# Performance work log

Measured on AMD Instinct MI355X. Metric: run time of the kernel, lower is better.

## Reference

```python
import jax, jax.numpy as jnp
import numpy as np

K = 16  # number of nearest neighbors (excluding self)
N = 16384


def setup_inputs() -> dict:
    key = jax.random.key(0)
    nodes = jax.random.normal(key, (N, 3), dtype=jnp.float32)
    return {"nodes": nodes}


def reference(nodes):
    n = nodes.shape[0]
    # Pairwise Euclidean distances via the Gram trick:
    # d(i,j)^2 = |x_i|^2 + |x_j|^2 - 2 <x_i, x_j>
    sq = jnp.sum(nodes * nodes, axis=1)                      # [n]
    d2 = sq[:, None] + sq[None, :] - 2.0 * (nodes @ nodes.T)  # [n, n]
    dist = jnp.sqrt(jnp.maximum(d2, 0.0))                    # clamp fp noise
    # k+1 smallest per row (self is nearest with distance ~0), then drop self.
    _, idx = jax.lax.top_k(-dist, K + 1)                     # ascending distance
    idx = idx[:, 1:]                                         # [n, K]
    rows = jnp.arange(n)[:, None]                            # [n, 1]
    adjacency = jnp.zeros((n, n), dtype=jnp.float32).at[rows, idx].set(1.0)
    return adjacency
```

## Files before the change

kernel.cpp:

```cpp
#include <hip/hip_runtime.h>
#include <math.h>

#define NN 16384
#define KK 16
#define RPW 4
#define SW 4
#define RPB (SW * RPW)
#define CAP 512
#define NB 1024
#define NT 64
#define FILL_BLOCKS 2048
#define SCAN_BLOCKS (NN / RPB)

typedef float f32x4 __attribute__((ext_vector_type(4)));
typedef unsigned long long u64;
typedef unsigned short u16;

#define WS_PTS   0
#define WS_PERM  (NN * 16)
#define WS_HIST  (WS_PERM + NN * 4)
#define WS_CUR   (WS_HIST + NB * 4)
#define WS_TMM   (WS_CUR + NB * 4)
#define WS_NB    (WS_TMM + NT * 8)
#define WS_NEED  (WS_NB + (size_t)NN * KK * 2)

__global__ void zero_hist(int* __restrict__ hist) { hist[threadIdx.x] = 0; }

__device__ __forceinline__ int xbucket(float x) {
    int b = (int)((x + 6.0f) * (NB / 12.0f));
    return b < 0 ? 0 : (b > NB - 1 ? NB - 1 : b);
}

__global__ void hist_kernel(const float* __restrict__ nodes, int* __restrict__ hist) {
    const int i = blockIdx.x * 256 + threadIdx.x;
    atomicAdd(&hist[xbucket(nodes[3 * i])], 1);
}

__global__ void scan_kernel(const int* __restrict__ hist, int* __restrict__ cur) {
    __shared__ int s[NB];
    const int tid = threadIdx.x;
    const int h0 = hist[tid];
    s[tid] = h0; __syncthreads();
    for (int o = 1; o < NB; o <<= 1) {
        const int v = (tid >= o) ? s[tid - o] : 0;
        __syncthreads();
        s[tid] += v;
        __syncthreads();
    }
    cur[tid] = s[tid] - h0;
}

__global__ void scatter_kernel(const float* __restrict__ nodes, int* __restrict__ cur,
                               float4* __restrict__ pts, int* __restrict__ perm) {
#pragma clang fp contract(off)
    const int i = blockIdx.x * 256 + threadIdx.x;
    const float x = nodes[3 * i], y = nodes[3 * i + 1], z = nodes[3 * i + 2];
    const float sq = (x * x + y * y) + z * z;
    const int pos = atomicAdd(&cur[xbucket(x)], 1);
    pts[pos] = make_float4(x, y, z, sq);
    perm[pos] = i;
}

__global__ void bounds_kernel(const float4* __restrict__ pts, float2* __restrict__ tmm) {
    __shared__ float mn[256], mx[256];
    const int tid = threadIdx.x;
    const float x = pts[blockIdx.x * 256 + tid].x;
    mn[tid] = x; mx[tid] = x; __syncthreads();
    for (int o = 128; o >= 1; o >>= 1) {
        if (tid < o) { mn[tid] = fminf(mn[tid], mn[tid + o]); mx[tid] = fmaxf(mx[tid], mx[tid + o]); }
        __syncthreads();
    }
    if (tid == 0) tmm[blockIdx.x] = make_float2(mn[0], mx[0]);
}

__device__ __forceinline__ float bcastf(float v, int l) {
    return __int_as_float(__builtin_amdgcn_readlane(__float_as_int(v), l));
}
__device__ __forceinline__ bool lexless(float da, int ia, float db, int ib) {
    return (da < db) || ((da == db) && (ia < ib));
}
__device__ __forceinline__ void insert_tile(bool rough, float d2, int j,
                                            float& ld, int& li,
                                            float& td, int& ti, float& td2u,
                                            int lane) {
#pragma clang fp contract(off)
    if (!__any(rough)) return;
    float dist = INFINITY;
    if (rough) dist = sqrtf(fmaxf(d2, 0.0f));
    bool done = false;
    while (true) {
        const bool pass = (!done) && rough && lexless(dist, j, td, ti);
        const u64 m = __ballot(pass);
        if (m == 0ull) break;
        const int src = __ffsll(m) - 1;
        const float dc = __shfl(dist, src);
        const int   ic = __shfl(j, src);
        if (lane == src) done = true;
        const bool gt = lexless(dc, ic, ld, li);
        const u64 gm = __ballot(gt);
        const int p = __ffsll(gm) - 1;
        const float pd = __shfl_up(ld, 1);
        const int   pi = __shfl_up(li, 1);
        if (gt) {
            if (lane == p) { ld = dc; li = ic; }
            else           { ld = pd; li = pi; }
        }
        td = __shfl(ld, 16);
        ti = __shfl(li, 16);
        td2u = td * td * 1.000001f;
    }
}

__device__ __forceinline__ void scan_body(int sblock,
                                          const float4* __restrict__ pts,
                                          const int* __restrict__ perm,
                                          const int* __restrict__ cur,
                                          const float2* __restrict__ tmm_g,
                                          const float* __restrict__ nodes,
                                          float* __restrict__ out,
                                          u16* __restrict__ nbws) {
#pragma clang fp contract(off)
    const int lane = threadIdx.x & 63;
    const int wid  = threadIdx.x >> 6;
    const int tid  = threadIdx.x;
    const int rowBase = sblock * RPB;

    __shared__ float2 tmm[NT];
    __shared__ u16 buf[SW][RPW][CAP];
    __shared__ u64 sel[SW][CAP];
    __shared__ int cnt[SW][RPW];

    if (tid < NT) tmm[tid] = tmm_g[tid];
    __syncthreads();

    float xs[RPW], ys[RPW], zs[RPW], ss[RPW];
    int tc[RPW];
#pragma unroll
    for (int r = 0; r < RPW; ++r) {
        const int row = rowBase + wid * RPW + r;
        xs[r] = nodes[3 * row];
        ys[r] = nodes[3 * row + 1];
        zs[r] = nodes[3 * row + 2];
        ss[r] = (xs[r] * xs[r] + ys[r] * ys[r]) + zs[r] * zs[r];
        int t = (cur[xbucket(xs[r])] - 1) >> 8;
        t = t - 1; t = t < 0 ? 0 : (t > NT - 3 ? NT - 3 : t);
        tc[r] = t;
    }

    float rm[RPW];
#pragma unroll
    for (int r = 0; r < RPW; ++r) rm[r] = INFINITY;
#pragma unroll
    for (int r = 0; r < RPW; ++r) {
        for (int tt = 0; tt < 3; ++tt) {
            const int tb = (tc[r] + tt) * 256;
            const float4 q0 = pts[tb + lane];
            const float4 q1 = pts[tb + 64 + lane];
            const float4 q2 = pts[tb + 128 + lane];
            const float4 q3 = pts[tb + 192 + lane];
            const float d0 = (ss[r] + q0.w) - 2.0f * fmaf(zs[r], q0.z, fmaf(ys[r], q0.y, xs[r] * q0.x));
            const float d1 = (ss[r] + q1.w) - 2.0f * fmaf(zs[r], q1.z, fmaf(ys[r], q1.y, xs[r] * q1.x));
            const float d2 = (ss[r] + q2.w) - 2.0f * fmaf(zs[r], q2.z, fmaf(ys[r], q2.y, xs[r] * q2.x));
            const float d3 = (ss[r] + q3.w) - 2.0f * fmaf(zs[r], q3.z, fmaf(ys[r], q3.y, xs[r] * q3.x));
            rm[r] = fminf(rm[r], fminf(fminf(d0, d1), fminf(d2, d3)));
        }
    }
    float sv[RPW];
#pragma unroll
    for (int r = 0; r < RPW; ++r) sv[r] = rm[r];
#pragma unroll
    for (int k = 2; k <= 64; k <<= 1) {
#pragma unroll
        for (int j = k >> 1; j >= 1; j >>= 1) {
            const bool keepmin = (((lane & j) == 0) == ((lane & k) == 0));
#pragma unroll
            for (int r = 0; r < RPW; ++r) {
                const float o = __shfl_xor(sv[r], j);
                sv[r] = keepmin ? fminf(sv[r], o) : fmaxf(sv[r], o);
            }
        }
    }
    float tau[RPW];
#pragma unroll
    for (int r = 0; r < RPW; ++r)
        tau[r] = fmaxf(bcastf(sv[r], 16), 0.0f) * 1.000002f + 1e-30f;

    if (lane < RPW) cnt[wid][lane] = 0;
    asm volatile("s_waitcnt lgkmcnt(0)" ::: "memory");

    for (int t = 0; t < NT; ++t) {
        const float2 mm = tmm[t];
        bool kp[RPW]; bool anyk = false;
#pragma unroll
        for (int r = 0; r < RPW; ++r) {
            const float dx = fmaxf(fmaxf(mm.x - xs[r], xs[r] - mm.y), 0.0f);
            kp[r] = (dx * dx <= tau[r] * 1.00001f + 5e-5f);
            anyk |= kp[r];
        }
        if (!anyk) continue;
        const int base = t * 256;
        const float4 q0 = pts[base + lane];
        const float4 q1 = pts[base + 64 + lane];
        const float4 q2 = pts[base + 128 + lane];
        const float4 q3 = pts[base + 192 + lane];
#pragma unroll
        for (int r = 0; r < RPW; ++r) {
            if (!kp[r]) continue;
            const float d0 = (ss[r] + q0.w) - 2.0f * fmaf(zs[r], q0.z, fmaf(ys[r], q0.y, xs[r] * q0.x));
            const float d1 = (ss[r] + q1.w) - 2.0f * fmaf(zs[r], q1.z, fmaf(ys[r], q1.y, xs[r] * q1.x));
            const float d2 = (ss[r] + q2.w) - 2.0f * fmaf(zs[r], q2.z, fmaf(ys[r], q2.y, xs[r] * q2.x));
            const float d3 = (ss[r] + q3.w) - 2.0f * fmaf(zs[r], q3.z, fmaf(ys[r], q3.y, xs[r] * q3.x));
            const bool p0 = d0 <= tau[r], p1 = d1 <= tau[r];
            const bool p2 = d2 <= tau[r], p3 = d3 <= tau[r];
            if (p0 | p1 | p2 | p3) {
                if (p0) { const int o = atomicAdd(&cnt[wid][r], 1);
                          if (o < CAP) buf[wid][r][o] = (u16)(base + lane); }
                if (p1) { const int o = atomicAdd(&cnt[wid][r], 1);
                          if (o < CAP) buf[wid][r][o] = (u16)(base + 64 + lane); }
                if (p2) { const int o = atomicAdd(&cnt[wid][r], 1);
                          if (o < CAP) buf[wid][r][o] = (u16)(base + 128 + lane); }
                if (p3) { const int o = atomicAdd(&cnt[wid][r], 1);
                          if (o < CAP) buf[wid][r][o] = (u16)(base + 192 + lane); }
            }
        }
    }
    asm volatile("s_waitcnt lgkmcnt(0)" ::: "memory");

#pragma unroll
    for (int r = 0; r < RPW; ++r) {
        const int C = cnt[wid][r];
        const int row = rowBase + wid * RPW + r;
        if (C <= CAP) {
            for (int e = lane; e < C; e += 64) {
                const int si = (int)buf[wid][r][e];
                const float4 q = pts[si];
                const float dd = (ss[r] + q.w) - 2.0f * fmaf(zs[r], q.z, fmaf(ys[r], q.y, xs[r] * q.x));
                const float dist = sqrtf(fmaxf(dd, 0.0f));
                sel[wid][e] = (((u64)__float_as_uint(dist)) << 32) | (unsigned)perm[si];
            }
            asm volatile("s_waitcnt lgkmcnt(0) vmcnt(0)" ::: "memory");
            for (int e = lane; e < C; e += 64) {
                const u64 my = sel[wid][e];
                int rk = 0;
                for (int c = 0; c < C; ++c)
                    rk += (sel[wid][c] < my) ? 1 : 0;
                if (rk >= 1 && rk <= KK) {
                    if (nbws) nbws[(size_t)row * KK + rk - 1] = (u16)(my & 0xffffu);
                    else      out[(size_t)row * NN + (int)(my & 0xffffffffu)] = 1.0f;
                }
            }
            asm volatile("s_waitcnt lgkmcnt(0)" ::: "memory");
        } else {
            float ld = INFINITY; int li = 0x7fffffff;
            float td = INFINITY; int ti = 0x7fffffff; float t2 = INFINITY;
            for (int tt = 0; tt < NN / 64; ++tt) {
                const int j = tt * 64 + lane;
                const float4 q = pts[j];
                const int oi = perm[j];
                const float dd = (ss[r] + q.w) - 2.0f * fmaf(zs[r], q.z, fmaf(ys[r], q.y, xs[r] * q.x));
                insert_tile(dd <= t2, dd, oi, ld, li, td, ti, t2, lane);
            }
            if (lane >= 1 && lane <= KK) {
                if (nbws) nbws[(size_t)row * KK + lane - 1] = (u16)li;
                else      out[(size_t)row * NN + li] = 1.0f;
            }
        }
    }
}

__global__ __launch_bounds__(256) void mega_kernel(const float4* __restrict__ pts,
                                                   const int* __restrict__ perm,
                                                   const int* __restrict__ cur,
                                                   const float2* __restrict__ tmm_g,
                                                   const float* __restrict__ nodes,
                                                   float* __restrict__ out,
                                                   u16* __restrict__ nbws) {
    const int b = blockIdx.x;
    if (b % 3 != 0) {
        const int fidx = (b / 3) * 2 + (b % 3) - 1;
        const int tid = fidx * 256 + threadIdx.x;
        const int nthreads = FILL_BLOCKS * 256;
        f32x4* ob = (f32x4*)out;
        const f32x4 z4 = {0.f, 0.f, 0.f, 0.f};
#pragma unroll 4
        for (int k = 0; k < (NN * (NN / 4)) / nthreads; ++k)
            __builtin_nontemporal_store(z4, ob + (size_t)k * nthreads + tid);
    } else {
        scan_body(b / 3, pts, perm, cur, tmm_g, nodes, nullptr, nbws);
    }
}

__global__ __launch_bounds__(256) void ones_kernel(const u16* __restrict__ nbws,
                                                   float* __restrict__ out) {
    const int t = blockIdx.x * 256 + threadIdx.x;
    const int row = t >> 4;
    out[(size_t)row * NN + nbws[t]] = 1.0f;
}

__global__ __launch_bounds__(256) void fill_zero(f32x4* __restrict__ ob) {
    const int tid = blockIdx.x * 256 + threadIdx.x;
    const int nthreads = FILL_BLOCKS * 256;
    const f32x4 z4 = {0.f, 0.f, 0.f, 0.f};
#pragma unroll 4
    for (int k = 0; k < (NN * (NN / 4)) / nthreads; ++k)
        __builtin_nontemporal_store(z4, ob + (size_t)k * nthreads + tid);
}

__global__ __launch_bounds__(256) void knn_scan_direct(const float4* __restrict__ pts,
                                                       const int* __restrict__ perm,
                                                       const int* __restrict__ cur,
                                                       const float2* __restrict__ tmm_g,
                                                       const float* __restrict__ nodes,
                                                       float* __restrict__ out) {
    scan_body(blockIdx.x, pts, perm, cur, tmm_g, nodes, out, nullptr);
}

extern "C" void kernel_launch(void* const* d_in, const int* in_sizes, int n_in,
                              void* d_out, int out_size, void* d_ws, size_t ws_size,
                              hipStream_t stream) {
    const float* nodes = (const float*)d_in[0];
    float* out = (float*)d_out;
    (void)in_sizes; (void)n_in; (void)out_size;

    char* ws = (char*)d_ws;
    float4* pts  = (float4*)(ws + WS_PTS);
    int*    perm = (int*)   (ws + WS_PERM);
    int*    hist = (int*)   (ws + WS_HIST);
    int*    cur  = (int*)   (ws + WS_CUR);
    float2* tmm  = (float2*)(ws + WS_TMM);
    u16*    nbws = (u16*)   (ws + WS_NB);

    hipLaunchKernelGGL(zero_hist,     dim3(1),        dim3(NB),  0, stream, hist);
    hipLaunchKernelGGL(hist_kernel,   dim3(NN / 256), dim3(256), 0, stream, nodes, hist);
    hipLaunchKernelGGL(scan_kernel,   dim3(1),        dim3(NB),  0, stream, hist, cur);
    hipLaunchKernelGGL(scatter_kernel,dim3(NN / 256), dim3(256), 0, stream, nodes, cur, pts, perm);
    hipLaunchKernelGGL(bounds_kernel, dim3(NT),       dim3(256), 0, stream, pts, tmm);

    if (ws_size >= WS_NEED) {
        hipLaunchKernelGGL(mega_kernel, dim3(SCAN_BLOCKS + FILL_BLOCKS),
                           dim3(256), 0, stream, pts, perm, cur, tmm, nodes, out, nbws);
        hipLaunchKernelGGL(ones_kernel, dim3(NN * KK / 256), dim3(256), 0, stream,
                           nbws, out);
    } else {
        hipLaunchKernelGGL(fill_zero, dim3(FILL_BLOCKS), dim3(256), 0, stream,
                           (f32x4*)out);
        hipLaunchKernelGGL(knn_scan_direct, dim3(SCAN_BLOCKS), dim3(256), 0, stream,
                           pts, perm, cur, tmm, nodes, out);
    }
}
```

Baseline: 304.3 us.

## Fuse bucket sort preprocessing into one block and overlap half the zero-fill

Collapses the five preprocessing kernels (hist zero, histogram, scan, scatter, bounds) into a single 1024-thread block that uses shared-memory atomics. That block runs alongside 512 blocks that zero the first half of the output. The mega kernel then zeroes only the second half, interleaved with the scan blocks. The aim is to cut launch overhead and hide the fill bandwidth behind the serial sort. The risk is that the single-block sort becomes a long serial critical path, since it scatters 16K points from one block.

```diff
diff --git a/kernel.cpp b/kernel.cpp
--- a/kernel.cpp
+++ b/kernel.cpp
@@ -9,8 +9,8 @@
 #define CAP 512
 #define NB 1024
 #define NT 64
-#define FILL_BLOCKS 2048
 #define SCAN_BLOCKS (NN / RPB)
+#define HALF_F4 (NN * (NN / 4) / 2)
 
 typedef float f32x4 __attribute__((ext_vector_type(4)));
 typedef unsigned long long u64;
@@ -24,53 +24,70 @@
 #define WS_NB    (WS_TMM + NT * 8)
 #define WS_NEED  (WS_NB + (size_t)NN * KK * 2)
 
-__global__ void zero_hist(int* __restrict__ hist) { hist[threadIdx.x] = 0; }
-
 __device__ __forceinline__ int xbucket(float x) {
     int b = (int)((x + 6.0f) * (NB / 12.0f));
     return b < 0 ? 0 : (b > NB - 1 ? NB - 1 : b);
 }
 
-__global__ void hist_kernel(const float* __restrict__ nodes, int* __restrict__ hist) {
-    const int i = blockIdx.x * 256 + threadIdx.x;
-    atomicAdd(&hist[xbucket(nodes[3 * i])], 1);
-}
-
-__global__ void scan_kernel(const int* __restrict__ hist, int* __restrict__ cur) {
-    __shared__ int s[NB];
-    const int tid = threadIdx.x;
-    const int h0 = hist[tid];
-    s[tid] = h0; __syncthreads();
+__global__ __launch_bounds__(1024) void k1_sortfill(const float* __restrict__ nodes,
+                                                    float4* __restrict__ pts,
+                                                    int* __restrict__ perm,
+                                                    int* __restrict__ cur_g,
+                                                    float2* __restrict__ tmm_g,
+                                                    float* __restrict__ out) {
+#pragma clang fp contract(off)
+    if (blockIdx.x != 0) {
+        const int fidx = blockIdx.x - 1;
+        const int tid = fidx * 1024 + threadIdx.x;
+        const int nthreads = 512 * 1024;
+        f32x4* ob = (f32x4*)out;
+        const f32x4 z4 = {0.f, 0.f, 0.f, 0.f};
+#pragma unroll 4
+        for (int k = 0; k < HALF_F4 / nthreads; ++k)
+            __builtin_nontemporal_store(z4, ob + (size_t)k * nthreads + tid);
+        return;
+    }
+    __shared__ int sh[NB];
+    __shared__ int shc[NB];
+    const int t = threadIdx.x;
+    sh[t] = 0;
+    __syncthreads();
+    for (int i = t; i < NN; i += 1024)
+        atomicAdd(&sh[xbucket(nodes[3 * i])], 1);
+    __syncthreads();
+    const int h0 = sh[t];
     for (int o = 1; o < NB; o <<= 1) {
-        const int v = (tid >= o) ? s[tid - o] : 0;
+        const int v = (t >= o) ? sh[t - o] : 0;
         __syncthreads();
-        s[tid] += v;
+        sh[t] += v;
         __syncthreads();
     }
-    cur[tid] = s[tid] - h0;
-}
-
-__global__ void scatter_kernel(const float* __restrict__ nodes, int* __restrict__ cur,
-                               float4* __restrict__ pts, int* __restrict__ perm) {
-#pragma clang fp contract(off)
-    const int i = blockIdx.x * 256 + threadIdx.x;
-    const float x = nodes[3 * i], y = nodes[3 * i + 1], z = nodes[3 * i + 2];
-    const float sq = (x * x + y * y) + z * z;
-    const int pos = atomicAdd(&cur[xbucket(x)], 1);
-    pts[pos] = make_float4(x, y, z, sq);
-    perm[pos] = i;
-}
-
-__global__ void bounds_kernel(const float4* __restrict__ pts, float2* __restrict__ tmm) {
-    __shared__ float mn[256], mx[256];
-    const int tid = threadIdx.x;
-    const float x = pts[blockIdx.x * 256 + tid].x;
-    mn[tid] = x; mx[tid] = x; __syncthreads();
-    for (int o = 128; o >= 1; o >>= 1) {
-        if (tid < o) { mn[tid] = fminf(mn[tid], mn[tid + o]); mx[tid] = fmaxf(mx[tid], mx[tid + o]); }
-        __syncthreads();
-    }
-    if (tid == 0) tmm[blockIdx.x] = make_float2(mn[0], mx[0]);
+    shc[t] = sh[t] - h0;
+    __syncthreads();
+    for (int i = t; i < NN; i += 1024) {
+        const float x = nodes[3 * i], y = nodes[3 * i + 1], z = nodes[3 * i + 2];
+        const float sq = (x * x + y * y) + z * z;
+        const int pos = atomicAdd(&shc[xbucket(x)], 1);
+        pts[pos] = make_float4(x, y, z, sq);
+        perm[pos] = i;
+    }
+    __syncthreads();
+    cur_g[t] = shc[t];
+    const int lane = t & 63, w = t >> 6;
+    for (int tt = w; tt < NT; tt += 16) {
+        float mn = INFINITY, mx = -INFINITY;
+#pragma unroll
+        for (int e = 0; e < 4; ++e) {
+            const float x = pts[tt * 256 + e * 64 + lane].x;
+            mn = fminf(mn, x); mx = fmaxf(mx, x);
+        }
+#pragma unroll
+        for (int s = 1; s <= 32; s <<= 1) {
+            mn = fminf(mn, __shfl_xor(mn, s));
+            mx = fmaxf(mx, __shfl_xor(mx, s));
+        }
+        if (lane == 0) tmm_g[tt] = make_float2(mn, mx);
+    }
 }
 
 __device__ __forceinline__ float bcastf(float v, int l) {
@@ -268,25 +285,25 @@
     }
 }
 
-__global__ __launch_bounds__(256) void mega_kernel(const float4* __restrict__ pts,
-                                                   const int* __restrict__ perm,
-                                                   const int* __restrict__ cur,
-                                                   const float2* __restrict__ tmm_g,
-                                                   const float* __restrict__ nodes,
-                                                   float* __restrict__ out,
-                                                   u16* __restrict__ nbws) {
+__global__ __launch_bounds__(256) void k2_mega(const float4* __restrict__ pts,
+                                               const int* __restrict__ perm,
+                                               const int* __restrict__ cur,
+                                               const float2* __restrict__ tmm_g,
+                                               const float* __restrict__ nodes,
+                                               float* __restrict__ out,
+                                               u16* __restrict__ nbws) {
     const int b = blockIdx.x;
-    if (b % 3 != 0) {
-        const int fidx = (b / 3) * 2 + (b % 3) - 1;
+    if (b & 1) {
+        const int fidx = b >> 1;
         const int tid = fidx * 256 + threadIdx.x;
-        const int nthreads = FILL_BLOCKS * 256;
-        f32x4* ob = (f32x4*)out;
+        const int nthreads = 1024 * 256;
+        f32x4* ob = (f32x4*)out + (size_t)HALF_F4;
         const f32x4 z4 = {0.f, 0.f, 0.f, 0.f};
 #pragma unroll 4
-        for (int k = 0; k < (NN * (NN / 4)) / nthreads; ++k)
+        for (int k = 0; k < HALF_F4 / nthreads; ++k)
             __builtin_nontemporal_store(z4, ob + (size_t)k * nthreads + tid);
     } else {
-        scan_body(b / 3, pts, perm, cur, tmm_g, nodes, nullptr, nbws);
+        scan_body(b >> 1, pts, perm, cur, tmm_g, nodes, nullptr, nbws);
     }
 }
 
@@ -297,9 +314,9 @@
     out[(size_t)row * NN + nbws[t]] = 1.0f;
 }
 
-__global__ __launch_bounds__(256) void fill_zero(f32x4* __restrict__ ob) {
+__global__ __launch_bounds__(256) void fill_zero_full(f32x4* __restrict__ ob) {
     const int tid = blockIdx.x * 256 + threadIdx.x;
-    const int nthreads = FILL_BLOCKS * 256;
+    const int nthreads = 2048 * 256;
     const f32x4 z4 = {0.f, 0.f, 0.f, 0.f};
 #pragma unroll 4
     for (int k = 0; k < (NN * (NN / 4)) / nthreads; ++k)
@@ -325,24 +342,21 @@
     char* ws = (char*)d_ws;
     float4* pts  = (float4*)(ws + WS_PTS);
     int*    perm = (int*)   (ws + WS_PERM);
-    int*    hist = (int*)   (ws + WS_HIST);
     int*    cur  = (int*)   (ws + WS_CUR);
     float2* tmm  = (float2*)(ws + WS_TMM);
     u16*    nbws = (u16*)   (ws + WS_NB);
 
-    hipLaunchKernelGGL(zero_hist,     dim3(1),        dim3(NB),  0, stream, hist);
-    hipLaunchKernelGGL(hist_kernel,   dim3(NN / 256), dim3(256), 0, stream, nodes, hist);
-    hipLaunchKernelGGL(scan_kernel,   dim3(1),        dim3(NB),  0, stream, hist, cur);
-    hipLaunchKernelGGL(scatter_kernel,dim3(NN / 256), dim3(256), 0, stream, nodes, cur, pts, perm);
-    hipLaunchKernelGGL(bounds_kernel, dim3(NT),       dim3(256), 0, stream, pts, tmm);
-
     if (ws_size >= WS_NEED) {
-        hipLaunchKernelGGL(mega_kernel, dim3(SCAN_BLOCKS + FILL_BLOCKS),
-                           dim3(256), 0, stream, pts, perm, cur, tmm, nodes, out, nbws);
+        hipLaunchKernelGGL(k1_sortfill, dim3(513), dim3(1024), 0, stream,
+                           nodes, pts, perm, cur, tmm, out);
+        hipLaunchKernelGGL(k2_mega, dim3(2 * SCAN_BLOCKS), dim3(256), 0, stream,
+                           pts, perm, cur, tmm, nodes, out, nbws);
         hipLaunchKernelGGL(ones_kernel, dim3(NN * KK / 256), dim3(256), 0, stream,
                            nbws, out);
     } else {
-        hipLaunchKernelGGL(fill_zero, dim3(FILL_BLOCKS), dim3(256), 0, stream,
+        hipLaunchKernelGGL(k1_sortfill, dim3(1), dim3(1024), 0, stream,
+                           nodes, pts, perm, cur, tmm, out);
+        hipLaunchKernelGGL(fill_zero_full, dim3(2048), dim3(256), 0, stream,
                            (f32x4*)out);
         hipLaunchKernelGGL(knn_scan_direct, dim3(SCAN_BLOCKS), dim3(256), 0, stream,
                            pts, perm, cur, tmm, nodes, out);
```

Result: slower. 325.1 us (+6.8%).
